# Kernel tuning notes

Measured on AMD Instinct MI355X. Metric: run time of the kernel, lower is better.

The kernel has to match this reference:

```python
import jax, jax.numpy as jnp
import numpy as np

# Dimensions (match init_kwargs / input_specs)
N, D, H, W, C = 2, 32, 32, 32, 128
G = 8                      # groups
Cg = C // G                # channels per group (16)
KS = 3                     # 3D kernel size
K = KS * KS * KS           # 27 sampling points per group (remove_center=False)
PAD, STRIDE, DIL = 1, 1, 1
OFFSET_SCALE = 1.0
OM_DIM = int(np.ceil(G * K * 4 / 8) * 8)  # 864 == G*K*4, no padding needed


def setup_inputs() -> dict:
    key = jax.random.key(0)
    ks = jax.random.split(key, 8)
    s = 1.0 / np.sqrt(C)
    return {
        "input": jax.random.normal(ks[0], (N, D, H, W, C), jnp.float32),
        "value_w": jax.random.normal(ks[1], (C, C), jnp.float32) * s,
        "value_b": jnp.zeros((C,), jnp.float32),
        # small offset/mask projection so sampling offsets stay near the kernel grid
        "offmask_w": jax.random.normal(ks[2], (OM_DIM, C), jnp.float32) * 0.01,
        "offmask_b": jax.random.normal(ks[3], (OM_DIM,), jnp.float32) * 0.01,
        "out_w": jax.random.normal(ks[4], (C, C), jnp.float32) * s,
        "out_b": jnp.zeros((C,), jnp.float32),
    }


def _dcnv4_core(x, offset_mask):
    """x: [N, L, G, Cg] value features. offset_mask: [N, L, OM_DIM].
    Per group / per point layout: K*3 offsets (d,h,w interleaved per point), then K masks.
    DCNv4 applies the mask WITHOUT softmax normalization.
    """
    L = D * H * W
    om = offset_mask[..., : G * K * 4].reshape(N, L, G, K * 4)
    offsets = om[..., : K * 3].reshape(N, L, G, K, 3)   # (d,h,w) offset per point
    masks = om[..., K * 3:]                              # [N, L, G, K]

    dz, hy, wx = jnp.meshgrid(jnp.arange(D), jnp.arange(H), jnp.arange(W), indexing="ij")
    base = jnp.stack([dz, hy, wx], -1).reshape(L, 3).astype(x.dtype) * STRIDE   # [L,3]
    kd, kh, kw = jnp.meshgrid(jnp.arange(KS), jnp.arange(KS), jnp.arange(KS), indexing="ij")
    kern = jnp.stack([kd, kh, kw], -1).reshape(K, 3).astype(x.dtype) * DIL - PAD  # [K,3]

    # sampling positions: [N, L, G, K, 3]
    pos = base[None, :, None, None, :] + kern[None, None, None, :, :] + offsets * OFFSET_SCALE

    vt = jnp.transpose(x, (0, 2, 1, 3))            # [N, G, L, Cg] for per-group gather
    sizes = jnp.array([D, H, W], x.dtype)

    def step(acc, pm):
        p, m = pm                                   # p: [N,L,G,3], m: [N,L,G]
        p0 = jnp.floor(p)
        t = p - p0                                  # trilinear fractions
        samp = jnp.zeros_like(acc)                  # [N, L, G, Cg]
        for cz in (0, 1):                           # 8 corners (fixed unroll)
            for cy in (0, 1):
                for cx in (0, 1):
                    c = p0 + jnp.array([cz, cy, cx], p.dtype)
                    wgt = ((t[..., 0] if cz else 1 - t[..., 0])
                           * (t[..., 1] if cy else 1 - t[..., 1])
                           * (t[..., 2] if cx else 1 - t[..., 2]))
                    valid = jnp.all((c >= 0) & (c < sizes), axis=-1)      # zero padding
                    ci = jnp.clip(c, 0, sizes - 1).astype(jnp.int32)
                    flat = (ci[..., 0] * H + ci[..., 1]) * W + ci[..., 2]  # [N,L,G]
                    idx = jnp.transpose(flat, (0, 2, 1))[..., None]        # [N,G,L,1]
                    g = jnp.take_along_axis(vt, idx, axis=2)               # [N,G,L,Cg]
                    g = jnp.transpose(g, (0, 2, 1, 3))                     # [N,L,G,Cg]
                    samp = samp + g * (wgt * valid)[..., None]
        return acc + samp * m[..., None], None

    pos_k = jnp.moveaxis(pos, 3, 0)    # [K, N, L, G, 3]
    mask_k = jnp.moveaxis(masks, 3, 0) # [K, N, L, G]
    out, _ = jax.lax.scan(step, jnp.zeros((N, L, G, Cg), x.dtype), (pos_k, mask_k))
    return out.reshape(N, L, C)


def reference(input, value_w, value_b, offmask_w, offmask_b, out_w, out_b):
    L = D * H * W
    xi = input.reshape(N, L, C)
    x = xi @ value_w.T + value_b             # value_proj
    om = xi @ offmask_w.T + offmask_b        # offset_mask projection (from raw input)
    out = _dcnv4_core(x.reshape(N, L, G, Cg), om)
    out = out @ out_w.T + out_b              # output_proj
    return out.reshape(N, D, H, W, C)
```

## Files before the change

kernel.cpp:

```cpp
#include <hip/hip_runtime.h>


typedef _Float16 f16;
typedef _Float16 f16x8 __attribute__((ext_vector_type(8)));
typedef _Float16 f16x4 __attribute__((ext_vector_type(4)));
typedef _Float16 f16x2 __attribute__((ext_vector_type(2)));
typedef float    f32x4 __attribute__((ext_vector_type(4)));

#define NB 2
#define DIM 32
#define CC 128
#define GG 8
#define CG 16
#define KPTS 27
#define LL (DIM*DIM*DIM)
#define MM (NB*LL)
#define OMD 864
#define PXW (CC + OMD)

#define SZV 96
#define SXV 8
#define PLANE 772

#define BST 152

__device__ __forceinline__ f16x2 pkrtz(float a, float b) {
  return __builtin_bit_cast(f16x2, __builtin_amdgcn_cvt_pkrtz(a, b));
}

__global__ __launch_bounds__(256) void build_wcat(const float* __restrict__ vw,
                                                  const float* __restrict__ ow,
                                                  f16* __restrict__ wcat) {
  int t = blockIdx.x * 256 + threadIdx.x;
  if (t >= PXW * 32) return;
  int p = t >> 5, c4 = (t & 31) * 4;
  const float* src;
  if (p < CC) {
    src = vw + (size_t)p * CC;
  } else {
    int q = p - CC, g = q / 108, r = q % 108, k = r >> 2, j = r & 3;
    src = ow + (size_t)(g * 108 + (j < 3 ? k * 3 + j : 81 + k)) * CC;
  }
  float4 v = *(const float4*)(src + c4);
  f16x4 o = {(f16)v.x, (f16)v.y, (f16)v.z, (f16)v.w};
  *(f16x4*)(wcat + (size_t)p * CC + c4) = o;
}

__global__ __launch_bounds__(256) void build_bias(const float* __restrict__ vb,
                                                  const float* __restrict__ ob,
                                                  float* __restrict__ pbias) {
  int p = blockIdx.x * 256 + threadIdx.x;
  if (p >= PXW) return;
  float v;
  if (p < CC) v = vb[p];
  else {
    int q = p - CC, g = q / 108, r = q % 108, k = r >> 2, j = r & 3;
    v = ob[g * 108 + (j < 3 ? k * 3 + j : 81 + k)];
  }
  pbias[p] = v;
}

__global__ __launch_bounds__(256) void cvt_f2h(const float* __restrict__ in,
                                               f16* __restrict__ out, int n4) {
  int i = blockIdx.x * blockDim.x + threadIdx.x;
  if (i >= n4) return;
  float4 v = ((const float4*)in)[i];
  f16x4 o = {(f16)v.x, (f16)v.y, (f16)v.z, (f16)v.w};
  ((f16x4*)out)[i] = o;
}

__global__ __launch_bounds__(256) void gemm_proj(
    const float* __restrict__ A, const f16* __restrict__ B,
    const float* __restrict__ bias, f16* __restrict__ xg,
    f16* __restrict__ om) {
  __shared__ f16 bs[2][32 * BST];
  __shared__ f16 tr[4][16 * 40];
  const int tid  = threadIdx.x;
  const int w    = tid >> 6;
  const int lane = tid & 63;
  const int rowBase = blockIdx.x * 64 + w * 16;
  const int r  = lane & 15;
  const int kg = lane >> 4;

  f16x8 a[4];
  {
    const float* Ap = A + (size_t)(rowBase + r) * CC + kg * 8;
#pragma unroll
    for (int kk = 0; kk < 4; ++kk) {
      float4 lo = *(const float4*)(Ap + kk * 32);
      float4 hi = *(const float4*)(Ap + kk * 32 + 4);
      f16x8 t;
      t[0] = (f16)lo.x; t[1] = (f16)lo.y; t[2] = (f16)lo.z; t[3] = (f16)lo.w;
      t[4] = (f16)hi.x; t[5] = (f16)hi.y; t[6] = (f16)hi.z; t[7] = (f16)hi.w;
      a[kk] = t;
    }
  }

  uint4 stg0, stg1;
  const int i0 = tid, i1 = tid + 256;
  const int d0 = (i0 >> 4) * BST + (i0 & 15) * 8;
  const int d1 = (i1 >> 4) * BST + (i1 & 15) * 8;

  {
    const f16* src = B;
    stg0 = *(const uint4*)(src + i0 * 8);
    stg1 = *(const uint4*)(src + i1 * 8);
    *(uint4*)(bs[0] + d0) = stg0;
    *(uint4*)(bs[0] + d1) = stg1;
  }
  __syncthreads();

  f16* tw = tr[w];
  for (int ct = 0; ct < 31; ++ct) {
    const int buf = ct & 1;
    if (ct + 1 < 31) {
      const f16* src = B + (ct + 1) * 4096;
      stg0 = *(const uint4*)(src + i0 * 8);
      stg1 = *(const uint4*)(src + i1 * 8);
    }
    const f16* bp = bs[buf];
    f32x4 acc0 = {0.f, 0.f, 0.f, 0.f};
    f32x4 acc1 = {0.f, 0.f, 0.f, 0.f};
#pragma unroll
    for (int kk = 0; kk < 4; ++kk) {
      f16x8 b0 = *(const f16x8*)(bp + r * BST + kg * 8 + kk * 32);
      f16x8 b1 = *(const f16x8*)(bp + (r + 16) * BST + kg * 8 + kk * 32);
      acc0 = __builtin_amdgcn_mfma_f32_16x16x32_f16(a[kk], b0, acc0, 0, 0, 0);
      acc1 = __builtin_amdgcn_mfma_f32_16x16x32_f16(a[kk], b1, acc1, 0, 0, 0);
    }
    const int colBase = ct * 32;
    const float bv0 = bias[colBase + r];
    const float bv1 = bias[colBase + 16 + r];
#pragma unroll
    for (int i = 0; i < 4; ++i) {
      const int trow = kg * 4 + i;
      tw[trow * 40 + r]      = (f16)(acc0[i] + bv0);
      tw[trow * 40 + 16 + r] = (f16)(acc1[i] + bv1);
    }
    asm volatile("s_waitcnt lgkmcnt(0)" ::: "memory");
    const int lrow = lane >> 2;
    const int c8   = (lane & 3) * 8;
    uint4 val = *(const uint4*)(tw + lrow * 40 + c8);
    const int row  = rowBase + lrow;
    if (ct < 4) {
      const int nn = row >> 15, flat = row & (LL - 1);
      const int g  = ct * 2 + ((lane >> 1) & 1);
      unsigned e = ((unsigned)((g * 2 + nn) << 15) + flat) * 16 + (lane & 1) * 8;
      *(uint4*)(xg + e) = val;
    } else {
      const int q0 = ct * 8 - 32 + (lane & 3) * 2;
      uint2 s0, s1;
      s0.x = val.x; s0.y = val.y;
      s1.x = val.z; s1.y = val.w;
      *(uint2*)(om + ((size_t)q0 * MM + row) * 4)       = s0;
      *(uint2*)(om + ((size_t)(q0 + 1) * MM + row) * 4) = s1;
    }
    asm volatile("s_waitcnt lgkmcnt(0)" ::: "memory");
    if (ct + 1 < 31) {
      *(uint4*)(bs[buf ^ 1] + d0) = stg0;
      *(uint4*)(bs[buf ^ 1] + d1) = stg1;
    }
    __syncthreads();
  }
}

__global__ __launch_bounds__(256) void gemm_out(
    const f16* __restrict__ Ain, const f16* __restrict__ B,
    const float* __restrict__ bias, float* __restrict__ fout) {
  const int w    = threadIdx.x >> 6;
  const int lane = threadIdx.x & 63;
  const int rowBase = blockIdx.x * 64 + w * 16;
  const int r  = lane & 15;
  const int kg = lane >> 4;
  const int ctBegin = blockIdx.y * 2;

  f16x8 a[4];
  const f16* A = Ain + (size_t)(rowBase + r) * CC + kg * 8;
#pragma unroll
  for (int kk = 0; kk < 4; ++kk) a[kk] = *(const f16x8*)(A + kk * 32);

  f16x8 bb[2][8];
#pragma unroll
  for (int s = 0; s < 2; ++s) {
    const f16* Bp = B + (unsigned)((ctBegin + s) * 32 + r) * CC + kg * 8;
#pragma unroll
    for (int kk = 0; kk < 4; ++kk) {
      bb[s][kk]     = *(const f16x8*)(Bp + kk * 32);
      bb[s][4 + kk] = *(const f16x8*)(Bp + 16 * CC + kk * 32);
    }
  }

#pragma unroll
  for (int t = 0; t < 2; ++t) {
    const int colBase = (ctBegin + t) * 32;
    f32x4 acc0 = {0.f, 0.f, 0.f, 0.f};
    f32x4 acc1 = {0.f, 0.f, 0.f, 0.f};
#pragma unroll
    for (int kk = 0; kk < 4; ++kk) {
      acc0 = __builtin_amdgcn_mfma_f32_16x16x32_f16(a[kk], bb[t][kk], acc0, 0, 0, 0);
      acc1 = __builtin_amdgcn_mfma_f32_16x16x32_f16(a[kk], bb[t][4 + kk], acc1, 0, 0, 0);
    }
    const float bv0 = bias[colBase + r];
    const float bv1 = bias[colBase + 16 + r];
    const int drow = rowBase + kg * 4;
    const int c0 = colBase + r, c1 = c0 + 16;
#pragma unroll
    for (int i = 0; i < 4; ++i) {
      unsigned ro = (unsigned)(drow + i) * CC;
      fout[ro + c0] = acc0[i] + bv0;
      fout[ro + c1] = acc1[i] + bv1;
    }
  }
}

__global__ __launch_bounds__(256) void dcn_core(const f16* __restrict__ xg,
                                                const f16* __restrict__ om,
                                                f16* __restrict__ y) {
  __shared__ uint4 ldsx[2 * PLANE];

  const int tid = threadIdx.x;
  int bid = blockIdx.x;
  const int g   = bid & 7;        bid >>= 3;
  const int n   = bid & 1;        bid >>= 1;
  const int tx0 = (bid & 3) * 8;  bid >>= 2;
  const int ty0 = (bid & 7) * 4;  bid >>= 3;
  const int tz0 = bid * 4;

  const f16* xgb = xg + (((size_t)(g * 2 + n)) << 15) * 16;
#pragma unroll
  for (int it = 0; it < 3; ++it) {
    int v = tid + it * 256;
    int lz = v / 96, r96 = v - lz * 96;
    int ly = r96 / 12, lx = r96 - ly * 12;
    int gz = tz0 - 2 + lz, gy = ty0 - 2 + ly, gx = tx0 - 2 + lx;
    uint4 d0 = {0u, 0u, 0u, 0u}, d1 = {0u, 0u, 0u, 0u};
    if (((unsigned)gz < DIM) & ((unsigned)gy < DIM) & ((unsigned)gx < DIM)) {
      const uint4* src = (const uint4*)(xgb + (size_t)(((gz << 5) + gy) * 32 + gx) * 16);
      d0 = src[0];
      d1 = src[1];
    }
    int vv = lz * SZV + lx * SXV + ly;
    ldsx[vv]         = d0;
    ldsx[PLANE + vv] = d1;
  }
  __syncthreads();

  const int wv   = tid >> 6;
  const int lane = tid & 63;
  const int pl   = lane >> 1;
  const int chd  = lane & 1;
  const int pz = wv, py = pl >> 3, px = pl & 7;
  const int dz = tz0 + pz, dy = ty0 + py, dx = tx0 + px;
  const unsigned row = (unsigned)(n << 15) + ((dz << 10) + (dy << 5) + dx);

  const int zoff = tz0 - 2, yoff = ty0 - 2, xoff = tx0 - 2;
  const int chbase = chd * PLANE;
  const int pb = g * 27;

  float dyf[3], dxf[3];
#pragma unroll
  for (int t = 0; t < 3; ++t) { dyf[t] = (float)(dy + t - 1); dxf[t] = (float)(dx + t - 1); }

  f16x2 acc0 = {(f16)0, (f16)0}, acc1 = acc0, acc2 = acc0, acc3 = acc0;
  const float CL = 0.99902344f;

  for (int kz = 0; kz < 3; ++kz) {
    const float bzf = (float)(dz + kz - 1);
    uint2 o[9];
#pragma unroll
    for (int j = 0; j < 9; ++j)
      o[j] = *(const uint2*)(om + ((size_t)(pb + kz * 9 + j) * MM + row) * 4);
#pragma unroll
    for (int j = 0; j < 9; ++j) {
      const int kh = j / 3, kw = j % 3;
      f16x2 o01 = __builtin_bit_cast(f16x2, o[j].x);
      f16x2 o23 = __builtin_bit_cast(f16x2, o[j].y);
      float od = fminf(fmaxf((float)o01[0], -CL), CL);
      float oh = fminf(fmaxf((float)o01[1], -CL), CL);
      float ow = fminf(fmaxf((float)o23[0], -CL), CL);
      float m  = (float)o23[1];
      float pd = bzf + od;
      float ph = dyf[kh] + oh;
      float pw = dxf[kw] + ow;
      float fd = floorf(pd), fh = floorf(ph), fw = floorf(pw);
      float td = pd - fd, th = ph - fh, tw = pw - fw;
      int id = (int)fd, ih = (int)fh, iw = (int)fw;
      float wz0 = (1.f - td) * m, wz1 = td * m;
      float wy0 = 1.f - th,        wy1 = th;
      float wx0 = 1.f - tw,        wx1 = tw;
      int az0 = (id - zoff) * SZV, az1 = az0 + SZV;
      int ay0 = (ih - yoff) + chbase, ay1 = ay0 + 1;
      int ax0 = (iw - xoff) * SXV, ax1 = ax0 + SXV;
      float wzy00 = wz0 * wy0, wzy01 = wz0 * wy1;
      float wzy10 = wz1 * wy0, wzy11 = wz1 * wy1;
#pragma unroll
      for (int c = 0; c < 8; ++c) {
        int idx = ((c & 4) ? az1 : az0) + ((c & 2) ? ay1 : ay0) + ((c & 1) ? ax1 : ax0);
        float wg = ((c & 4) ? ((c & 2) ? wzy11 : wzy10)
                            : ((c & 2) ? wzy01 : wzy00)) * ((c & 1) ? wx1 : wx0);
        uint4 q = ldsx[idx];
        f16x2 w2 = pkrtz(wg, wg);
        acc0 = __builtin_bit_cast(f16x2, q.x) * w2 + acc0;
        acc1 = __builtin_bit_cast(f16x2, q.y) * w2 + acc1;
        acc2 = __builtin_bit_cast(f16x2, q.z) * w2 + acc2;
        acc3 = __builtin_bit_cast(f16x2, q.w) * w2 + acc3;
      }
    }
  }

  uint4 st;
  st.x = __builtin_bit_cast(unsigned, acc0);
  st.y = __builtin_bit_cast(unsigned, acc1);
  st.z = __builtin_bit_cast(unsigned, acc2);
  st.w = __builtin_bit_cast(unsigned, acc3);
  *(uint4*)(y + (size_t)row * CC + g * CG + chd * 8) = st;
}

extern "C" void kernel_launch(void* const* d_in, const int* in_sizes, int n_in,
                              void* d_out, int out_size, void* d_ws, size_t ws_size,
                              hipStream_t stream) {
  const float* f_in      = (const float*)d_in[0];
  const float* value_w   = (const float*)d_in[1];
  const float* value_b   = (const float*)d_in[2];
  const float* offmask_w = (const float*)d_in[3];
  const float* offmask_b = (const float*)d_in[4];
  const float* out_w     = (const float*)d_in[5];
  const float* out_b     = (const float*)d_in[6];
  float* out = (float*)d_out;

  f16* wcat = (f16*)d_ws;
  f16* wout = wcat + (size_t)PXW * CC;
  f16* xg   = wout + (size_t)CC * CC;
  f16* om   = xg + (size_t)GG * NB * LL * CG;
  f16* y    = om + (size_t)216 * MM * 4;
  float* pbias = (float*)(y + (size_t)MM * CC);

  build_wcat<<<(PXW * 32 + 255) / 256, 256, 0, stream>>>(value_w, offmask_w, wcat);
  build_bias<<<(PXW + 255) / 256, 256, 0, stream>>>(value_b, offmask_b, pbias);
  cvt_f2h<<<(CC * CC / 4 + 255) / 256, 256, 0, stream>>>(out_w, wout, CC * CC / 4);

  gemm_proj<<<MM / 64, dim3(256), 0, stream>>>(f_in, wcat, pbias, xg, om);
  dcn_core<<<4096, dim3(256), 0, stream>>>(xg, om, y);
  gemm_out<<<dim3(MM / 64, 2), dim3(256), 0, stream>>>(y, wout, out_b, out);
}
```

Measured before the change: 161.9 us.

## Fuse offset/mask projection into dcn_core via per-block MFMA into LDS

The offset/mask projection (864 columns) moves out of gemm_proj and into dcn_core. Each block computes its group's 108 columns for its 128 positions with MFMA and writes them to LDS, and gemm_proj now produces only the value projection. This removes the write and read of the large fp16 offset/mask intermediate in global memory. In exchange, each dcn block reloads raw fp32 input rows and weight tiles, and the LDS footprint grows, which may lower occupancy.

```diff
diff --git a/kernel.cpp b/kernel.cpp
--- a/kernel.cpp
+++ b/kernel.cpp
@@ -20,12 +20,20 @@
 
 #define SZV 96
 #define SXV 8
-#define PLANE 772
+#define PLANE 770
 
 #define BST 152
 
 __device__ __forceinline__ f16x2 pkrtz(float a, float b) {
   return __builtin_bit_cast(f16x2, __builtin_amdgcn_cvt_pkrtz(a, b));
+}
+__device__ __forceinline__ f16x8 cvt8(float4 lo, float4 hi) {
+  uint4 u;
+  u.x = __builtin_bit_cast(unsigned, pkrtz(lo.x, lo.y));
+  u.y = __builtin_bit_cast(unsigned, pkrtz(lo.z, lo.w));
+  u.z = __builtin_bit_cast(unsigned, pkrtz(hi.x, hi.y));
+  u.w = __builtin_bit_cast(unsigned, pkrtz(hi.z, hi.w));
+  return __builtin_bit_cast(f16x8, u);
 }
 
 __global__ __launch_bounds__(256) void build_wcat(const float* __restrict__ vw,
@@ -71,8 +79,7 @@
 
 __global__ __launch_bounds__(256) void gemm_proj(
     const float* __restrict__ A, const f16* __restrict__ B,
-    const float* __restrict__ bias, f16* __restrict__ xg,
-    f16* __restrict__ om) {
+    const float* __restrict__ bias, f16* __restrict__ xg) {
   __shared__ f16 bs[2][32 * BST];
   __shared__ f16 tr[4][16 * 40];
   const int tid  = threadIdx.x;
@@ -100,20 +107,18 @@
   const int i0 = tid, i1 = tid + 256;
   const int d0 = (i0 >> 4) * BST + (i0 & 15) * 8;
   const int d1 = (i1 >> 4) * BST + (i1 & 15) * 8;
-
   {
-    const f16* src = B;
-    stg0 = *(const uint4*)(src + i0 * 8);
-    stg1 = *(const uint4*)(src + i1 * 8);
+    stg0 = *(const uint4*)(B + i0 * 8);
+    stg1 = *(const uint4*)(B + i1 * 8);
     *(uint4*)(bs[0] + d0) = stg0;
     *(uint4*)(bs[0] + d1) = stg1;
   }
   __syncthreads();
 
   f16* tw = tr[w];
-  for (int ct = 0; ct < 31; ++ct) {
+  for (int ct = 0; ct < 4; ++ct) {
     const int buf = ct & 1;
-    if (ct + 1 < 31) {
+    if (ct + 1 < 4) {
       const f16* src = B + (ct + 1) * 4096;
       stg0 = *(const uint4*)(src + i0 * 8);
       stg1 = *(const uint4*)(src + i1 * 8);
@@ -142,21 +147,12 @@
     const int c8   = (lane & 3) * 8;
     uint4 val = *(const uint4*)(tw + lrow * 40 + c8);
     const int row  = rowBase + lrow;
-    if (ct < 4) {
-      const int nn = row >> 15, flat = row & (LL - 1);
-      const int g  = ct * 2 + ((lane >> 1) & 1);
-      unsigned e = ((unsigned)((g * 2 + nn) << 15) + flat) * 16 + (lane & 1) * 8;
-      *(uint4*)(xg + e) = val;
-    } else {
-      const int q0 = ct * 8 - 32 + (lane & 3) * 2;
-      uint2 s0, s1;
-      s0.x = val.x; s0.y = val.y;
-      s1.x = val.z; s1.y = val.w;
-      *(uint2*)(om + ((size_t)q0 * MM + row) * 4)       = s0;
-      *(uint2*)(om + ((size_t)(q0 + 1) * MM + row) * 4) = s1;
-    }
+    const int nn = row >> 15, flat = row & (LL - 1);
+    const int g  = ct * 2 + ((lane >> 1) & 1);
+    unsigned e = ((unsigned)((g * 2 + nn) << 15) + flat) * 16 + (lane & 1) * 8;
+    *(uint4*)(xg + e) = val;
     asm volatile("s_waitcnt lgkmcnt(0)" ::: "memory");
-    if (ct + 1 < 31) {
+    if (ct + 1 < 4) {
       *(uint4*)(bs[buf ^ 1] + d0) = stg0;
       *(uint4*)(bs[buf ^ 1] + d1) = stg1;
     }
@@ -213,10 +209,12 @@
   }
 }
 
-__global__ __launch_bounds__(256) void dcn_core(const f16* __restrict__ xg,
-                                                const f16* __restrict__ om,
-                                                f16* __restrict__ y) {
+__global__ __launch_bounds__(256) void dcn_core(
+    const float* __restrict__ xi, const f16* __restrict__ wcat,
+    const float* __restrict__ pbias, const f16* __restrict__ xg,
+    f16* __restrict__ y) {
   __shared__ uint4 ldsx[2 * PLANE];
+  __shared__ uint2 ldsom[28 * 128];
 
   const int tid = threadIdx.x;
   int bid = blockIdx.x;
@@ -225,6 +223,9 @@
   const int tx0 = (bid & 3) * 8;  bid >>= 2;
   const int ty0 = (bid & 7) * 4;  bid >>= 3;
   const int tz0 = bid * 4;
+
+  const int lane = tid & 63;
+  const int wv   = tid >> 6;
 
   const f16* xgb = xg + (((size_t)(g * 2 + n)) << 15) * 16;
 #pragma unroll
@@ -243,19 +244,59 @@
     ldsx[vv]         = d0;
     ldsx[PLANE + vv] = d1;
   }
+
+  {
+    const int r  = lane & 15;
+    const int kg = lane >> 4;
+    f16x8 bfr[2][4];
+#pragma unroll
+    for (int pt = 0; pt < 2; ++pt) {
+      const int posi = (wv * 2 + pt) * 16 + r;
+      const int pz = posi >> 5, py = (posi >> 3) & 3, px = posi & 7;
+      const float* xr = xi + ((size_t)(n << 15) + ((tz0 + pz) << 10) +
+                              ((ty0 + py) << 5) + (tx0 + px)) * CC + kg * 8;
+#pragma unroll
+      for (int kk = 0; kk < 4; ++kk) {
+        float4 lo = *(const float4*)(xr + kk * 32);
+        float4 hi = *(const float4*)(xr + kk * 32 + 4);
+        bfr[pt][kk] = cvt8(lo, hi);
+      }
+    }
+    const f16* wg_ = wcat + (size_t)(CC + g * 108) * CC;
+    const float* bb = pbias + CC + g * 108;
+#pragma unroll
+    for (int mt = 0; mt < 7; ++mt) {
+      f16x8 afr[4];
+      const f16* ar = wg_ + (size_t)(mt * 16 + r) * CC + kg * 8;
+#pragma unroll
+      for (int kk = 0; kk < 4; ++kk) afr[kk] = *(const f16x8*)(ar + kk * 32);
+      float4 bv = *(const float4*)(bb + mt * 16 + kg * 4);
+      const int krow = mt * 4 + kg;
+#pragma unroll
+      for (int pt = 0; pt < 2; ++pt) {
+        f32x4 acc = {0.f, 0.f, 0.f, 0.f};
+#pragma unroll
+        for (int kk = 0; kk < 4; ++kk)
+          acc = __builtin_amdgcn_mfma_f32_16x16x32_f16(afr[kk], bfr[pt][kk], acc, 0, 0, 0);
+        const int posw = (wv * 2 + pt) * 16 + r;
+        uint2 val;
+        val.x = __builtin_bit_cast(unsigned, pkrtz(acc[0] + bv.x, acc[1] + bv.y));
+        val.y = __builtin_bit_cast(unsigned, pkrtz(acc[2] + bv.z, acc[3] + bv.w));
+        ldsom[krow * 128 + posw] = val;
+      }
+    }
+  }
   __syncthreads();
 
-  const int wv   = tid >> 6;
-  const int lane = tid & 63;
   const int pl   = lane >> 1;
   const int chd  = lane & 1;
+  const int posi = wv * 32 + pl;
   const int pz = wv, py = pl >> 3, px = pl & 7;
   const int dz = tz0 + pz, dy = ty0 + py, dx = tx0 + px;
   const unsigned row = (unsigned)(n << 15) + ((dz << 10) + (dy << 5) + dx);
 
   const int zoff = tz0 - 2, yoff = ty0 - 2, xoff = tx0 - 2;
   const int chbase = chd * PLANE;
-  const int pb = g * 27;
 
   float dyf[3], dxf[3];
 #pragma unroll
@@ -269,7 +310,7 @@
     uint2 o[9];
 #pragma unroll
     for (int j = 0; j < 9; ++j)
-      o[j] = *(const uint2*)(om + ((size_t)(pb + kz * 9 + j) * MM + row) * 4);
+      o[j] = ldsom[(kz * 9 + j) * 128 + posi];
 #pragma unroll
     for (int j = 0; j < 9; ++j) {
       const int kh = j / 3, kw = j % 3;
@@ -331,15 +372,14 @@
   f16* wcat = (f16*)d_ws;
   f16* wout = wcat + (size_t)PXW * CC;
   f16* xg   = wout + (size_t)CC * CC;
-  f16* om   = xg + (size_t)GG * NB * LL * CG;
-  f16* y    = om + (size_t)216 * MM * 4;
+  f16* y    = xg + (size_t)GG * NB * LL * CG;
   float* pbias = (float*)(y + (size_t)MM * CC);
 
   build_wcat<<<(PXW * 32 + 255) / 256, 256, 0, stream>>>(value_w, offmask_w, wcat);
   build_bias<<<(PXW + 255) / 256, 256, 0, stream>>>(value_b, offmask_b, pbias);
   cvt_f2h<<<(CC * CC / 4 + 255) / 256, 256, 0, stream>>>(out_w, wout, CC * CC / 4);
 
-  gemm_proj<<<MM / 64, dim3(256), 0, stream>>>(f_in, wcat, pbias, xg, om);
-  dcn_core<<<4096, dim3(256), 0, stream>>>(xg, om, y);
+  gemm_proj<<<MM / 64, dim3(256), 0, stream>>>(f_in, wcat, pbias, xg);
+  dcn_core<<<4096, dim3(256), 0, stream>>>(f_in, wcat, pbias, xg, y);
   gemm_out<<<dim3(MM / 64, 2), dim3(256), 0, stream>>>(y, wout, out_b, out);
 }
```

Measured after the change: 163.0 us. About the same (+0.7%).
